# Performance work log

Hardware: AMD Instinct MI355X
Metric: run time of the kernel (lower is better)

## Reference

```python
import jax, jax.numpy as jnp
from jax import lax
import numpy as np

B, N = 32, 16384
C, K = 64, 21
T = 30
L = 10.0
LAM = 0.1


def setup_inputs() -> dict:
    key = jax.random.key(0)
    k1, k2 = jax.random.split(key)
    y = jax.random.normal(k1, (B, 1, N), dtype=jnp.float32)
    H = jax.random.normal(k2, (C, 1, K), dtype=jnp.float32)
    H = H / jnp.linalg.norm(H, axis=-1, keepdims=True)  # F.normalize(p=2, dim=-1)
    return {"y": y, "H": H}


def _conv(y, H):
    # torch F.conv1d(y [B,1,N], H [C,1,K]) -> [B,C,N-K+1] (cross-correlation)
    return lax.conv_general_dilated(y, H, (1,), 'VALID',
                                    dimension_numbers=('NCH', 'OIH', 'NCH'))


def _convT(x, H):
    # torch F.conv_transpose1d(x [B,C,M], H [C,1,K]) -> [B,1,M+K-1]
    k = H.shape[-1]
    Ht = jnp.transpose(jnp.flip(H, -1), (1, 0, 2))  # [1,C,K] OIH, flipped
    return lax.conv_general_dilated(x, Ht, (1,), [(k - 1, k - 1)],
                                    dimension_numbers=('NCH', 'OIH', 'NCH'))


def reference(y, H):
    enc_dim = y.shape[-1] - H.shape[-1] + 1  # N - K + 1
    b = y.shape[0]
    c = H.shape[0]
    x0 = jnp.zeros((b, c, enc_dim), dtype=y.dtype)
    s0 = jnp.asarray(1.0, dtype=y.dtype)

    def step(carry, _):
        x_old, x_tmp, s_old = carry
        res = y - _convT(x_tmp, H)                      # residual [B,1,N]
        x_new = x_tmp + _conv(res, H) / L               # gradient step
        x_new = jax.nn.relu(x_new - LAM / L)            # soft-threshold (nonneg)
        s_new = (1.0 + jnp.sqrt(1.0 + 4.0 * s_old * s_old)) / 2.0
        x_tmp_next = x_new + (s_old - 1.0) / s_new * (x_new - x_old)
        return (x_new, x_tmp_next, s_new), None

    (x_new, _, _), _ = lax.scan(step, (x0, x0, s0), None, length=T)
    y_hat = _convT(x_new, H)
    return (y_hat, x_new)
```

## Files before the change

### kernel.cpp

```cpp
#include <hip/hip_runtime.h>
#include <math.h>

#define B_ 32
#define N_ 16384
#define K_ 21
#define C_ 64
#define M_ (N_ - K_ + 1)
#define T_ 30

#define TILE 236
#define NBLK 70
#define UPW  256
#define XRW  284
#define NT   256

__device__ __forceinline__ void wave_lds_fence() {
  asm volatile("" ::: "memory");
  __builtin_amdgcn_wave_barrier();
}

__global__ __launch_bounds__(NT) void fused_step2_kernel(
    const float* __restrict__ Xc, const float* __restrict__ Xo,
    float* __restrict__ Xw,
    const float* __restrict__ Ut, const float* __restrict__ Uo,
    float* __restrict__ Uw,
    const float* __restrict__ y, const float* __restrict__ Hg,
    const float bp, const float bm, const int first)
{
  __shared__ float rs[256];
  __shared__ float xr[16][XRW];
  __shared__ float rp[4][256];

  const int tid = threadIdx.x;
  const int wv  = tid >> 6;
  const int l   = tid & 63;
  const int b   = blockIdx.y;
  const int x   = blockIdx.x;
  const int m0  = x * TILE;
  const bool has_o = (bm != 0.f);

  {
    float4* p = (float4*)&xr[0][0];
    #pragma unroll
    for (int s = 0; s < 5; ++s) {
      const int idx = tid + (s << 8);
      if (idx < 16 * XRW / 4) p[idx] = make_float4(0.f, 0.f, 0.f, 0.f);
    }
  }

  {
    const int n = m0 + tid;
    float r = 0.f;
    if (n < N_) {
      r = y[(size_t)b * N_ + n];
      if (!first) {
        const float* Ub = Ut + (size_t)b * NBLK * UPW;
        float ut;
        if (tid >= 236) {
          ut = Ub[(x + 1) * UPW + tid - 236] + Ub[x * UPW + tid];
        } else {
          ut = Ub[x * UPW + tid];
          if (tid < 20 && x > 0) ut += Ub[(x - 1) * UPW + 236 + tid];
        }
        r -= bp * ut;
        if (has_o) {
          const float* Vb = Uo + (size_t)b * NBLK * UPW;
          float uo;
          if (tid >= 236) {
            uo = Vb[(x + 1) * UPW + tid - 236] + Vb[x * UPW + tid];
          } else {
            uo = Vb[x * UPW + tid];
            if (tid < 20 && x > 0) uo += Vb[(x - 1) * UPW + 236 + tid];
          }
          r -= bm * uo;
        }
      }
    }
    rs[tid] = r;
  }
  __syncthreads();

  const int rem = M_ - m0;
  const bool act = (l < 59) && ((l << 2) < rem);
  float p0 = 0.f, p1 = 0.f, p2 = 0.f, p3 = 0.f;

  for (int k = 0; k < 4; ++k) {
    if (act) {
      float wr[24];
      #pragma unroll
      for (int kk = 0; kk < 6; ++kk) {
        const float4 v = *(const float4*)&rs[(l << 2) + (kk << 2)];
        wr[4*kk+0] = v.x; wr[4*kk+1] = v.y;
        wr[4*kk+2] = v.z; wr[4*kk+3] = v.w;
      }
      #pragma unroll
      for (int j = 0; j < 4; ++j) {
        const int row = (wv << 2) + j;
        const int cg  = __builtin_amdgcn_readfirstlane((k << 4) + row);
        const size_t gro = ((size_t)b * C_ + cg) * M_ + m0 + (l << 2);
        float xt0 = 0.f, xt1 = 0.f, xt2 = 0.f, xt3 = 0.f;
        if (!first) {
          const float4 a = *(const float4*)(Xc + gro);
          float ox = 0.f, oy = 0.f, oz = 0.f, ow = 0.f;
          if (has_o) {
            const float4 o = *(const float4*)(Xo + gro);
            ox = o.x; oy = o.y; oz = o.z; ow = o.w;
          }
          xt0 = fmaf(bm, ox, bp * a.x);
          xt1 = fmaf(bm, oy, bp * a.y);
          xt2 = fmaf(bm, oz, bp * a.z);
          xt3 = fmaf(bm, ow, bp * a.w);
        }
        const float* hc = Hg + cg * K_;
        float g0 = 0.f, g1 = 0.f, g2 = 0.f, g3 = 0.f;
        #pragma unroll
        for (int u = 0; u < 21; ++u) {
          const float hv = hc[u];
          g0 = fmaf(wr[u],     hv, g0);
          g1 = fmaf(wr[u + 1], hv, g1);
          g2 = fmaf(wr[u + 2], hv, g2);
          g3 = fmaf(wr[u + 3], hv, g3);
        }
        const float o0 = fmaxf(fmaf(g0, 0.1f, xt0) - 0.01f, 0.f);
        const float o1 = fmaxf(fmaf(g1, 0.1f, xt1) - 0.01f, 0.f);
        const float o2 = fmaxf(fmaf(g2, 0.1f, xt2) - 0.01f, 0.f);
        const float o3 = fmaxf(fmaf(g3, 0.1f, xt3) - 0.01f, 0.f);
        *(float4*)(Xw + gro) = make_float4(o0, o1, o2, o3);
        *(float4*)&xr[row][20 + (l << 2)] = make_float4(o0, o1, o2, o3);
      }
    }
    wave_lds_fence();

    #pragma unroll
    for (int j = 0; j < 4; ++j) {
      const int row = (wv << 2) + j;
      const int cg  = __builtin_amdgcn_readfirstlane((k << 4) + row);
      const float* hc = Hg + cg * K_;
      float w[24];
      #pragma unroll
      for (int kk = 0; kk < 6; ++kk) {
        const float4 v = *(const float4*)&xr[row][(l << 2) + (kk << 2)];
        w[4*kk+0] = v.x; w[4*kk+1] = v.y;
        w[4*kk+2] = v.z; w[4*kk+3] = v.w;
      }
      #pragma unroll
      for (int u = 0; u < 21; ++u) {
        const float hv = hc[20 - u];
        p0 = fmaf(w[u],     hv, p0);
        p1 = fmaf(w[u + 1], hv, p1);
        p2 = fmaf(w[u + 2], hv, p2);
        p3 = fmaf(w[u + 3], hv, p3);
      }
    }
    wave_lds_fence();
  }

  rp[wv][(l<<2)+0] = p0; rp[wv][(l<<2)+1] = p1;
  rp[wv][(l<<2)+2] = p2; rp[wv][(l<<2)+3] = p3;
  __syncthreads();

  Uw[((size_t)b * NBLK + x) * UPW + tid] =
      rp[0][tid] + rp[1][tid] + rp[2][tid] + rp[3][tid];
}

__global__ __launch_bounds__(NT) void yhat_combine_kernel(
    const float* __restrict__ Uw, float* __restrict__ outy)
{
  const int tid = threadIdx.x;
  const int n = blockIdx.x * 256 + tid;
  const int b = blockIdx.y;
  const int x = n / 236;
  const int i = n - x * 236;
  const float* Ub = Uw + (size_t)b * NBLK * UPW;
  float v = Ub[x * UPW + i];
  if (i < 20 && x > 0) v += Ub[(x - 1) * UPW + 236 + i];
  outy[(size_t)b * N_ + n] = v;
}

#define XWID 276
#define Q4PC 69
#define NQ4  (16 * Q4PC)

__global__ __launch_bounds__(NT, 4) void fused_step_r5_kernel(
    const float* __restrict__ Xc, const float* __restrict__ Xo,
    float* __restrict__ Xw, const float* __restrict__ y,
    const float* __restrict__ Hg, const float bp, const float bm,
    const int first)
{
  __shared__ float xs[16][XWID];
  __shared__ float rp[4][256];
  __shared__ float rs[256];

  const int tid = threadIdx.x;
  const int wv  = tid >> 6;
  const int l   = tid & 63;
  const int b   = blockIdx.y;
  const int m0  = blockIdx.x * TILE;
  const int g0  = m0 - 20;
  const bool has_o = (bm != 0.f);

  if (!first) {
    float p0 = 0.f, p1 = 0.f, p2 = 0.f, p3 = 0.f;
    for (int k = 0; k < 4; ++k) {
      const int ch0 = k << 4;
      const float* pcb = Xc + ((size_t)b * C_ + ch0) * M_;
      const float* pob = Xo + ((size_t)b * C_ + ch0) * M_;
      __syncthreads();
      for (int f = tid; f < NQ4; f += NT) {
        const int c  = f / Q4PC;
        const int i4 = f - c * Q4PC;
        const int g  = g0 + (i4 << 2);
        const float* pa = pcb + (size_t)c * M_ + g;
        const float* pb = pob + (size_t)c * M_ + g;
        float ax, ay, az, aw, ox, oy, oz, ow;
        if (g >= 0 && g + 3 < M_) {
          const float4 a = *(const float4*)pa;
          ax = a.x; ay = a.y; az = a.z; aw = a.w;
          if (has_o) {
            const float4 o = *(const float4*)pb;
            ox = o.x; oy = o.y; oz = o.z; ow = o.w;
          } else { ox = oy = oz = ow = 0.f; }
        } else {
          ax = ay = az = aw = ox = oy = oz = ow = 0.f;
          if ((unsigned)(g+0) < (unsigned)M_) { ax = pa[0]; if (has_o) ox = pb[0]; }
          if ((unsigned)(g+1) < (unsigned)M_) { ay = pa[1]; if (has_o) oy = pb[1]; }
          if ((unsigned)(g+2) < (unsigned)M_) { az = pa[2]; if (has_o) oz = pb[2]; }
          if ((unsigned)(g+3) < (unsigned)M_) { aw = pa[3]; if (has_o) ow = pb[3]; }
        }
        float4 w4;
        w4.x = fmaf(bm, ox, bp * ax);
        w4.y = fmaf(bm, oy, bp * ay);
        w4.z = fmaf(bm, oz, bp * az);
        w4.w = fmaf(bm, ow, bp * aw);
        *(float4*)&xs[c][i4 << 2] = w4;
      }
      __syncthreads();
      #pragma unroll
      for (int j = 0; j < 4; ++j) {
        const int cloc = (wv << 2) + j;
        const int cg = __builtin_amdgcn_readfirstlane(ch0 + cloc);
        const float* hc = Hg + cg * K_;
        float w[24];
        #pragma unroll
        for (int kk = 0; kk < 6; ++kk) {
          const float4 v = *(const float4*)&xs[cloc][(l << 2) + (kk << 2)];
          w[4*kk+0] = v.x; w[4*kk+1] = v.y;
          w[4*kk+2] = v.z; w[4*kk+3] = v.w;
        }
        #pragma unroll
        for (int u = 0; u < 21; ++u) {
          const float hv = hc[20 - u];
          p0 = fmaf(w[u],     hv, p0);
          p1 = fmaf(w[u + 1], hv, p1);
          p2 = fmaf(w[u + 2], hv, p2);
          p3 = fmaf(w[u + 3], hv, p3);
        }
      }
    }
    *(float4*)&rp[wv][l << 2] = make_float4(p0, p1, p2, p3);
  }
  __syncthreads();

  {
    const int n = m0 + tid;
    float r = 0.f;
    if (n < N_) {
      r = y[(size_t)b * N_ + n];
      if (!first) r -= rp[0][tid] + rp[1][tid] + rp[2][tid] + rp[3][tid];
    }
    rs[tid] = r;
  }
  __syncthreads();

  if (l < 59 && (l << 2) < M_ - m0) {
    float wr[24];
    #pragma unroll
    for (int kk = 0; kk < 6; ++kk) {
      const float4 v = *(const float4*)&rs[(l << 2) + (kk << 2)];
      wr[4*kk+0] = v.x; wr[4*kk+1] = v.y;
      wr[4*kk+2] = v.z; wr[4*kk+3] = v.w;
    }
    #pragma unroll 4
    for (int cl = 0; cl < 16; ++cl) {
      const int cg = __builtin_amdgcn_readfirstlane((wv << 4) + cl);
      const size_t row = ((size_t)b * C_ + cg) * M_ + m0 + (l << 2);
      float xt0, xt1, xt2, xt3;
      if (!first) {
        const float4 a = *(const float4*)(Xc + row);
        float ox = 0.f, oy = 0.f, oz = 0.f, ow = 0.f;
        if (has_o) {
          const float4 o = *(const float4*)(Xo + row);
          ox = o.x; oy = o.y; oz = o.z; ow = o.w;
        }
        xt0 = fmaf(bm, ox, bp * a.x);
        xt1 = fmaf(bm, oy, bp * a.y);
        xt2 = fmaf(bm, oz, bp * a.z);
        xt3 = fmaf(bm, ow, bp * a.w);
      } else { xt0 = xt1 = xt2 = xt3 = 0.f; }
      const float* hc = Hg + cg * K_;
      float a0 = 0.f, a1 = 0.f, a2 = 0.f, a3 = 0.f;
      #pragma unroll
      for (int u = 0; u < 21; ++u) {
        const float hv = hc[u];
        a0 = fmaf(wr[u],     hv, a0);
        a1 = fmaf(wr[u + 1], hv, a1);
        a2 = fmaf(wr[u + 2], hv, a2);
        a3 = fmaf(wr[u + 3], hv, a3);
      }
      const float o0 = fmaxf(fmaf(a0, 0.1f, xt0) - 0.01f, 0.f);
      const float o1 = fmaxf(fmaf(a1, 0.1f, xt1) - 0.01f, 0.f);
      const float o2 = fmaxf(fmaf(a2, 0.1f, xt2) - 0.01f, 0.f);
      const float o3 = fmaxf(fmaf(a3, 0.1f, xt3) - 0.01f, 0.f);
      *(float4*)(Xw + row) = make_float4(o0, o1, o2, o3);
    }
  }
}

#define TA 1024
#define CC 16

__global__ __launch_bounds__(NT) void convT_kernel(
    const float* __restrict__ X, const float* __restrict__ y,
    const float* __restrict__ Hg, float* __restrict__ out,
    const int use_y, const float sign)
{
  __shared__ float xs[CC][TA + 20];
  __shared__ float hs[C_][K_];
  const int tid = threadIdx.x;
  const int b = blockIdx.y;
  const int n0 = blockIdx.x * TA;

  for (int f = tid; f < C_ * K_; f += NT) hs[f / K_][f % K_] = sign * Hg[f];

  float acc[4];
  if (use_y) {
    const float4 v = *(const float4*)(y + (size_t)b * N_ + n0 + tid * 4);
    acc[0] = v.x; acc[1] = v.y; acc[2] = v.z; acc[3] = v.w;
  } else {
    acc[0] = acc[1] = acc[2] = acc[3] = 0.f;
  }
  const bool interior = (n0 >= 20) && (n0 + TA - 1 <= M_ - 1);
  const int QROW = (TA + 20) / 4;
  for (int cb = 0; cb < C_; cb += CC) {
    __syncthreads();
    for (int f = tid; f < CC * QROW; f += NT) {
      const int c = f / QROW;
      const int i = (f % QROW) * 4;
      const int gx = n0 - 20 + i;
      const float* src = X + ((size_t)(b * C_ + cb + c)) * M_ + gx;
      float4 v;
      if (interior) {
        v = *(const float4*)src;
      } else {
        v.x = (gx >= 0     && gx < M_)     ? src[0] : 0.f;
        v.y = (gx + 1 >= 0 && gx + 1 < M_) ? src[1] : 0.f;
        v.z = (gx + 2 >= 0 && gx + 2 < M_) ? src[2] : 0.f;
        v.w = (gx + 3 >= 0 && gx + 3 < M_) ? src[3] : 0.f;
      }
      *(float4*)&xs[c][i] = v;
    }
    __syncthreads();
    for (int c = 0; c < CC; ++c) {
      float w[24];
      #pragma unroll
      for (int k = 0; k < 6; ++k) {
        const float4 v = *(const float4*)&xs[c][tid * 4 + k * 4];
        w[k*4] = v.x; w[k*4+1] = v.y; w[k*4+2] = v.z; w[k*4+3] = v.w;
      }
      const float* hr = hs[cb + c];
      #pragma unroll
      for (int j = 0; j < K_; ++j) {
        const float h = hr[j];
        acc[0] = fmaf(h, w[20 - j], acc[0]);
        acc[1] = fmaf(h, w[21 - j], acc[1]);
        acc[2] = fmaf(h, w[22 - j], acc[2]);
        acc[3] = fmaf(h, w[23 - j], acc[3]);
      }
    }
  }
  *(float4*)(out + (size_t)b * N_ + n0 + tid * 4) =
      make_float4(acc[0], acc[1], acc[2], acc[3]);
}

extern "C" void kernel_launch(void* const* d_in, const int* in_sizes, int n_in,
                              void* d_out, int out_size, void* d_ws, size_t ws_size,
                              hipStream_t stream)
{
  const float* y = (const float*)d_in[0];
  const float* H = (const float*)d_in[1];
  float* out  = (float*)d_out;
  float* outy = out;
  float* outx = out + (size_t)B_ * N_;

  const size_t SZ = (size_t)B_ * C_ * M_;
  const size_t UP = (size_t)B_ * NBLK * UPW;

  float betas[T_];
  double s = 1.0;
  for (int t = 0; t < T_; ++t) {
    const double sn = (1.0 + sqrt(1.0 + 4.0 * s * s)) * 0.5;
    betas[t] = (float)((s - 1.0) / sn);
    s = sn;
  }

  float* P[3] = { (float*)d_ws, (float*)d_ws + SZ, outx };
  const dim3 blk(NT);

  if (ws_size >= (2 * SZ + 3 * UP) * sizeof(float)) {
    float* U[3] = { (float*)d_ws + 2 * SZ,
                    (float*)d_ws + 2 * SZ + UP,
                    (float*)d_ws + 2 * SZ + 2 * UP };
    const dim3 gF(NBLK, B_);
    for (int t = 0; t < T_; ++t) {
      const float beta = (t >= 1) ? betas[t - 1] : 0.f;
      const float* Xc = P[(t + 2) % 3];
      const float* Xo = (beta != 0.f) ? P[(t + 1) % 3] : P[(t + 2) % 3];
      float*       Xw = P[t % 3];
      const float* Ut = U[(t + 2) % 3];
      const float* Uo = (beta != 0.f) ? U[(t + 1) % 3] : U[(t + 2) % 3];
      float*       Uw = U[t % 3];
      fused_step2_kernel<<<gF, blk, 0, stream>>>(
          Xc, Xo, Xw, Ut, Uo, Uw, y, H, 1.f + beta, -beta, t == 0);
    }
    const dim3 gY(N_ / 256, B_);
    yhat_combine_kernel<<<gY, blk, 0, stream>>>(U[(T_ - 1) % 3], outy);
  } else {
    const dim3 gF((M_ + TILE - 1) / TILE, B_);
    for (int t = 0; t < T_; ++t) {
      const float beta = (t >= 1) ? betas[t - 1] : 0.f;
      const float* Xc = P[(t + 2) % 3];
      const float* Xo = (beta != 0.f) ? P[(t + 1) % 3] : P[(t + 2) % 3];
      float*       Xw = P[t % 3];
      fused_step_r5_kernel<<<gF, blk, 0, stream>>>(Xc, Xo, Xw, y, H,
                                                   1.f + beta, -beta, t == 0);
    }
    const dim3 gA(N_ / TA, B_);
    convT_kernel<<<gA, blk, 0, stream>>>(outx, y, H, outy, 0, 1.f);
  }
}
```

Measured before the change: 2.873 ms.

## Software-pipeline Xc/Xo loads and reuse register outputs in fused FISTA step

Rewrites the fused step kernel so the four Xc/Xo row loads for the next channel chunk are issued before the LDS fence and the transpose-conv phase of the current chunk, hiding global memory latency. The residual window is hoisted out of the chunk loop, rs is padded so every lane can run unconditionally, and the last four taps of the transpose conv come from registers rather than being re-read from LDS. The loads now run even on the first step and when beta is zero, which adds some memory traffic, and the unrolled macros raise register pressure.

```diff
diff --git a/kernel.cpp b/kernel.cpp
--- a/kernel.cpp
+++ b/kernel.cpp
@@ -19,7 +19,86 @@
   __builtin_amdgcn_wave_barrier();
 }
 
-__global__ __launch_bounds__(NT) void fused_step2_kernel(
+#define LOADC(k)                                                            \
+  {                                                                         \
+    const float* pc_ = XcB + (size_t)((k) * 16 + (wv << 2)) * M_ + coff;    \
+    const float* po_ = XoB + (size_t)((k) * 16 + (wv << 2)) * M_ + coff;    \
+    la0 = *(const float4*)pc_;                                              \
+    lo0 = *(const float4*)po_;                                              \
+    la1 = *(const float4*)(pc_ + M_);                                       \
+    lo1 = *(const float4*)(po_ + M_);                                       \
+    la2 = *(const float4*)(pc_ + 2 * M_);                                   \
+    lo2 = *(const float4*)(po_ + 2 * M_);                                   \
+    la3 = *(const float4*)(pc_ + 3 * M_);                                   \
+    lo3 = *(const float4*)(po_ + 3 * M_);                                   \
+  }
+
+#define ROWA(k, j, la, lo, oo0, oo1, oo2, oo3)                              \
+  {                                                                         \
+    const int cg_ = __builtin_amdgcn_readfirstlane((k)*16 + (wv<<2) + (j)); \
+    const float* hc_ = Hg + cg_ * K_;                                       \
+    float g0_ = 0.f, g1_ = 0.f, g2_ = 0.f, g3_ = 0.f;                       \
+    _Pragma("unroll")                                                       \
+    for (int u_ = 0; u_ < 21; ++u_) {                                       \
+      const float hv_ = hc_[u_];                                            \
+      g0_ = fmaf(wr[u_],     hv_, g0_);                                     \
+      g1_ = fmaf(wr[u_ + 1], hv_, g1_);                                     \
+      g2_ = fmaf(wr[u_ + 2], hv_, g2_);                                     \
+      g3_ = fmaf(wr[u_ + 3], hv_, g3_);                                     \
+    }                                                                       \
+    const float xt0_ = first ? 0.f : fmaf(bm, lo.x, bp * la.x);             \
+    const float xt1_ = first ? 0.f : fmaf(bm, lo.y, bp * la.y);             \
+    const float xt2_ = first ? 0.f : fmaf(bm, lo.z, bp * la.z);             \
+    const float xt3_ = first ? 0.f : fmaf(bm, lo.w, bp * la.w);             \
+    oo0 = fmaxf(fmaf(g0_, 0.1f, xt0_) - 0.01f, 0.f);                        \
+    oo1 = fmaxf(fmaf(g1_, 0.1f, xt1_) - 0.01f, 0.f);                        \
+    oo2 = fmaxf(fmaf(g2_, 0.1f, xt2_) - 0.01f, 0.f);                        \
+    oo3 = fmaxf(fmaf(g3_, 0.1f, xt3_) - 0.01f, 0.f);                        \
+    if (!act) { oo0 = 0.f; oo1 = 0.f; oo2 = 0.f; oo3 = 0.f; }               \
+    if (act)                                                                \
+      *(float4*)(Xw + (bC + (k)*16 + (wv<<2) + (j)) * M_ + mown) =          \
+          make_float4(oo0, oo1, oo2, oo3);                                  \
+    *(float4*)&xr[(wv<<2) + (j)][20 + (l << 2)] =                           \
+        make_float4(oo0, oo1, oo2, oo3);                                    \
+  }
+
+#define ROWB(k, j, oo0, oo1, oo2, oo3)                                      \
+  {                                                                         \
+    const int cg_ = __builtin_amdgcn_readfirstlane((k)*16 + (wv<<2) + (j)); \
+    const float* hc_ = Hg + cg_ * K_;                                       \
+    float w_[24];                                                           \
+    _Pragma("unroll")                                                       \
+    for (int kk_ = 0; kk_ < 5; ++kk_) {                                     \
+      const float4 v_ =                                                     \
+          *(const float4*)&xr[(wv<<2) + (j)][(l << 2) + (kk_ << 2)];        \
+      w_[4*kk_+0] = v_.x; w_[4*kk_+1] = v_.y;                               \
+      w_[4*kk_+2] = v_.z; w_[4*kk_+3] = v_.w;                               \
+    }                                                                       \
+    w_[20] = oo0; w_[21] = oo1; w_[22] = oo2; w_[23] = oo3;                 \
+    _Pragma("unroll")                                                       \
+    for (int u_ = 0; u_ < 21; ++u_) {                                       \
+      const float hv_ = hc_[20 - u_];                                       \
+      p0 = fmaf(w_[u_],     hv_, p0);                                       \
+      p1 = fmaf(w_[u_ + 1], hv_, p1);                                       \
+      p2 = fmaf(w_[u_ + 2], hv_, p2);                                       \
+      p3 = fmaf(w_[u_ + 3], hv_, p3);                                       \
+    }                                                                       \
+  }
+
+#define CHUNK(k, PRE)                                                       \
+  ROWA(k, 0, la0, lo0, o00, o01, o02, o03)                                  \
+  ROWA(k, 1, la1, lo1, o10, o11, o12, o13)                                  \
+  ROWA(k, 2, la2, lo2, o20, o21, o22, o23)                                  \
+  ROWA(k, 3, la3, lo3, o30, o31, o32, o33)                                  \
+  PRE                                                                       \
+  wave_lds_fence();                                                         \
+  ROWB(k, 0, o00, o01, o02, o03)                                            \
+  ROWB(k, 1, o10, o11, o12, o13)                                            \
+  ROWB(k, 2, o20, o21, o22, o23)                                            \
+  ROWB(k, 3, o30, o31, o32, o33)                                            \
+  wave_lds_fence();
+
+__global__ __launch_bounds__(NT) void fused_step3_kernel(
     const float* __restrict__ Xc, const float* __restrict__ Xo,
     float* __restrict__ Xw,
     const float* __restrict__ Ut, const float* __restrict__ Uo,
@@ -27,7 +106,7 @@
     const float* __restrict__ y, const float* __restrict__ Hg,
     const float bp, const float bm, const int first)
 {
-  __shared__ float rs[256];
+  __shared__ float rs[280];
   __shared__ float xr[16][XRW];
   __shared__ float rp[4][256];
 
@@ -46,6 +125,7 @@
       const int idx = tid + (s << 8);
       if (idx < 16 * XRW / 4) p[idx] = make_float4(0.f, 0.f, 0.f, 0.f);
     }
+    if (tid < 24) rs[256 + tid] = 0.f;
   }
 
   {
@@ -80,80 +160,31 @@
   }
   __syncthreads();
 
-  const int rem = M_ - m0;
+  float wr[24];
+  #pragma unroll
+  for (int kk = 0; kk < 6; ++kk) {
+    const float4 v = *(const float4*)&rs[(l << 2) + (kk << 2)];
+    wr[4*kk+0] = v.x; wr[4*kk+1] = v.y;
+    wr[4*kk+2] = v.z; wr[4*kk+3] = v.w;
+  }
+
+  const int mown = m0 + (l << 2);
+  const int coff = (mown <= M_ - 4) ? mown : (M_ - 4);
+  const int rem  = M_ - m0;
   const bool act = (l < 59) && ((l << 2) < rem);
+  const size_t bC = (size_t)b * C_;
+  const float* XcB = Xc + bC * M_;
+  const float* XoB = Xo + bC * M_;
+
   float p0 = 0.f, p1 = 0.f, p2 = 0.f, p3 = 0.f;
-
-  for (int k = 0; k < 4; ++k) {
-    if (act) {
-      float wr[24];
-      #pragma unroll
-      for (int kk = 0; kk < 6; ++kk) {
-        const float4 v = *(const float4*)&rs[(l << 2) + (kk << 2)];
-        wr[4*kk+0] = v.x; wr[4*kk+1] = v.y;
-        wr[4*kk+2] = v.z; wr[4*kk+3] = v.w;
-      }
-      #pragma unroll
-      for (int j = 0; j < 4; ++j) {
-        const int row = (wv << 2) + j;
-        const int cg  = __builtin_amdgcn_readfirstlane((k << 4) + row);
-        const size_t gro = ((size_t)b * C_ + cg) * M_ + m0 + (l << 2);
-        float xt0 = 0.f, xt1 = 0.f, xt2 = 0.f, xt3 = 0.f;
-        if (!first) {
-          const float4 a = *(const float4*)(Xc + gro);
-          float ox = 0.f, oy = 0.f, oz = 0.f, ow = 0.f;
-          if (has_o) {
-            const float4 o = *(const float4*)(Xo + gro);
-            ox = o.x; oy = o.y; oz = o.z; ow = o.w;
-          }
-          xt0 = fmaf(bm, ox, bp * a.x);
-          xt1 = fmaf(bm, oy, bp * a.y);
-          xt2 = fmaf(bm, oz, bp * a.z);
-          xt3 = fmaf(bm, ow, bp * a.w);
-        }
-        const float* hc = Hg + cg * K_;
-        float g0 = 0.f, g1 = 0.f, g2 = 0.f, g3 = 0.f;
-        #pragma unroll
-        for (int u = 0; u < 21; ++u) {
-          const float hv = hc[u];
-          g0 = fmaf(wr[u],     hv, g0);
-          g1 = fmaf(wr[u + 1], hv, g1);
-          g2 = fmaf(wr[u + 2], hv, g2);
-          g3 = fmaf(wr[u + 3], hv, g3);
-        }
-        const float o0 = fmaxf(fmaf(g0, 0.1f, xt0) - 0.01f, 0.f);
-        const float o1 = fmaxf(fmaf(g1, 0.1f, xt1) - 0.01f, 0.f);
-        const float o2 = fmaxf(fmaf(g2, 0.1f, xt2) - 0.01f, 0.f);
-        const float o3 = fmaxf(fmaf(g3, 0.1f, xt3) - 0.01f, 0.f);
-        *(float4*)(Xw + gro) = make_float4(o0, o1, o2, o3);
-        *(float4*)&xr[row][20 + (l << 2)] = make_float4(o0, o1, o2, o3);
-      }
-    }
-    wave_lds_fence();
-
-    #pragma unroll
-    for (int j = 0; j < 4; ++j) {
-      const int row = (wv << 2) + j;
-      const int cg  = __builtin_amdgcn_readfirstlane((k << 4) + row);
-      const float* hc = Hg + cg * K_;
-      float w[24];
-      #pragma unroll
-      for (int kk = 0; kk < 6; ++kk) {
-        const float4 v = *(const float4*)&xr[row][(l << 2) + (kk << 2)];
-        w[4*kk+0] = v.x; w[4*kk+1] = v.y;
-        w[4*kk+2] = v.z; w[4*kk+3] = v.w;
-      }
-      #pragma unroll
-      for (int u = 0; u < 21; ++u) {
-        const float hv = hc[20 - u];
-        p0 = fmaf(w[u],     hv, p0);
-        p1 = fmaf(w[u + 1], hv, p1);
-        p2 = fmaf(w[u + 2], hv, p2);
-        p3 = fmaf(w[u + 3], hv, p3);
-      }
-    }
-    wave_lds_fence();
-  }
+  float4 la0, lo0, la1, lo1, la2, lo2, la3, lo3;
+  float o00,o01,o02,o03, o10,o11,o12,o13, o20,o21,o22,o23, o30,o31,o32,o33;
+
+  LOADC(0)
+  CHUNK(0, LOADC(1))
+  CHUNK(1, LOADC(2))
+  CHUNK(2, LOADC(3))
+  CHUNK(3, )
 
   rp[wv][(l<<2)+0] = p0; rp[wv][(l<<2)+1] = p1;
   rp[wv][(l<<2)+2] = p2; rp[wv][(l<<2)+3] = p3;
@@ -419,7 +450,7 @@
       const float* Ut = U[(t + 2) % 3];
       const float* Uo = (beta != 0.f) ? U[(t + 1) % 3] : U[(t + 2) % 3];
       float*       Uw = U[t % 3];
-      fused_step2_kernel<<<gF, blk, 0, stream>>>(
+      fused_step3_kernel<<<gF, blk, 0, stream>>>(
           Xc, Xo, Xw, Ut, Uo, Uw, y, H, 1.f + beta, -beta, t == 0);
     }
     const dim3 gY(N_ / 256, B_);
```

Measured after the change: 5.046 ms. 75.7% more time.
